# Kernel tuning notes

Measured on AMD Instinct MI355X. Metric: run time of the kernel, lower is better.

## Reference

```python
import jax, jax.numpy as jnp
import numpy as np

EPS = 1e-8
LN_EPS = 1e-5  # torch LayerNorm default


def _l2norm(x):
    # L2-norm along last dim, keepdim, clamped at 1e-8 (matches _l2_norm)
    return jnp.maximum(jnp.sqrt(jnp.sum(x * x, axis=-1, keepdims=True)), 1e-8)


def _ln(x, g, b, n_axes):
    # LayerNorm over the last n_axes dims with elementwise affine
    axes = tuple(range(x.ndim - n_axes, x.ndim))
    mu = jnp.mean(x, axis=axes, keepdims=True)
    var = jnp.var(x, axis=axes, keepdims=True)
    return (x - mu) / jnp.sqrt(var + LN_EPS) * g + b


def _get_zs(x, Wk, bk, Wv, bv, zg, zb, sg, sb):
    z = jax.nn.elu(x @ Wk + bk)                     # (B,L,D)
    v = x @ Wv + bv                                  # (B,L,D)
    s = jnp.einsum('blp,blq->blpq', z, v)            # (B,L,D,D)
    z = jnp.cumsum(z, axis=1)
    s = jnp.cumsum(s, axis=1)
    return _ln(z + EPS, zg, zb, 1), _ln(s + EPS, sg, sb, 2)


def setup_inputs() -> dict:
    key = jax.random.key(0)
    ks = jax.random.split(key, 16)
    B, L, LP, IN, D, NU = 16, 512, 8, 64, 64, 1024
    w = lambda k, sh: (jax.random.normal(k, sh, dtype=jnp.float32) * 0.05)
    inp = {
        'user_id': jax.random.randint(ks[0], (B,), 0, NU),
        'seqs_emb': jax.random.normal(ks[1], (B, L, IN), dtype=jnp.float32),
        'P': jax.random.normal(ks[2], (B, LP, IN), dtype=jnp.float32),
        'S': jax.random.normal(ks[3], (B, LP, IN), dtype=jnp.float32),
        'Wq': w(ks[4], (IN, D)), 'bq': jnp.zeros((D,), jnp.float32),
        'Wk': w(ks[5], (IN, D)), 'bk': jnp.zeros((D,), jnp.float32),
        'Wv': w(ks[6], (IN, D)), 'bv': jnp.zeros((D,), jnp.float32),
        'z_g': jnp.ones((D,), jnp.float32), 'z_b': jnp.zeros((D,), jnp.float32),
        's_g': jnp.ones((D, D), jnp.float32), 's_b': jnp.zeros((D, D), jnp.float32),
        'nam_g': jnp.ones((D, D), jnp.float32), 'nam_b': jnp.zeros((D, D), jnp.float32),
        'na_g': jnp.ones((D,), jnp.float32), 'na_b': jnp.zeros((D,), jnp.float32),
        'prev_z_buf': w(ks[7], (NU + 1, D)),
        'prev_s_buf': w(ks[8], (NU + 1, D, D)),
    }
    return inp


def reference(user_id, seqs_emb, P, S, Wq, bq, Wk, bk, Wv, bv,
              z_g, z_b, s_g, s_b, nam_g, nam_b, na_g, na_b,
              prev_z_buf, prev_s_buf):
    q = jax.nn.elu(seqs_emb @ Wq + bq)                          # (B,L,D)
    z, s = _get_zs(seqs_emb, Wk, bk, Wv, bv, z_g, z_b, s_g, s_b)
    # prompt P: add last-step cumulative state
    P_z, P_s = _get_zs(P, Wk, bk, Wv, bv, z_g, z_b, s_g, s_b)
    z = z + P_z[:, -1:, :]
    s = s + P_s[:, -1:, :, :]
    # CSN path (use_csn=True): q normalized with detached norm
    norm_q = q / jax.lax.stop_gradient(_l2norm(q))
    nam = s / _l2norm(z)[..., None]                             # (B,L,D,D)
    na = jnp.einsum('bld,bldp->blp', norm_q, _ln(nam + EPS, nam_g, nam_b, 2))
    # history path (use_history=True) with prompt S
    S_z, S_s = _get_zs(S, Wk, bk, Wv, bv, z_g, z_b, s_g, s_b)
    prev_z = prev_z_buf[user_id] + S_z[:, -1, :]                # (B,D)
    prev_s = prev_s_buf[user_id] + S_s[:, -1, :, :]             # (B,D,D)
    prev_nam = prev_s / (_l2norm(prev_z)[..., None] + EPS)
    prev_na = jnp.einsum('blp,bpq->blq', norm_q, _ln(prev_nam + EPS, nam_g, nam_b, 2))
    na = na + prev_na  # dropout is identity in eval mode
    na = _ln(na, na_g, na_b, 1)
    # unbiased std over all elements (torch.std default)
    std = jnp.std(q / jnp.maximum(z, 1e-6), ddof=1)
    return na, std
```

## Files before the change

### kernel.cpp

```cpp
#include <hip/hip_runtime.h>
#include <math.h>
#include <stdint.h>

#define B_ 16
#define L_ 512
#define IN_ 64
#define D_ 64
#define LP_ 8

#define LN_EPS 1e-5f
#define EPSF 1e-8f

__device__ __forceinline__ float wredf(float v){
    #pragma unroll
    for (int o = 32; o; o >>= 1) v += __shfl_xor(v, o, 64);
    return v;
}
__device__ __forceinline__ double wredd(double v){
    #pragma unroll
    for (int o = 32; o; o >>= 1) v += __shfl_xor(v, o, 64);
    return v;
}

__device__ __forceinline__ void gl_lds4(const float* gsrc, float* ldst){
    __builtin_amdgcn_global_load_lds((const __attribute__((address_space(1))) void*)gsrc,
                                     (__attribute__((address_space(3))) void*)ldst, 4, 0, 0);
}

template<int LC, int NCH>
__global__ __launch_bounds__(256) void k0_fused(
    const float* __restrict__ X,
    const float* __restrict__ Wq, const float* __restrict__ bq,
    const float* __restrict__ Wk, const float* __restrict__ bk,
    const float* __restrict__ Wv, const float* __restrict__ bv,
    float* __restrict__ Q, float* __restrict__ Z, float* __restrict__ V,
    float* __restrict__ spart, float* __restrict__ zpart,
    double* __restrict__ qstats)
{
    __shared__ float sW[3][IN_*D_];
    __shared__ float sx[4][IN_];
    __shared__ float sz[16][D_], sv[16][D_];
    int t = threadIdx.x;
    if (blockIdx.x == 0 && t < 2) qstats[t] = 0.0;
    for (int i = t; i < IN_*D_; i += 256){ sW[0][i]=Wq[i]; sW[1][i]=Wk[i]; sW[2][i]=Wv[i]; }
    int p = t & 63, g = t >> 6;
    float bqv = bq[p], bkv = bk[p], bvv = bv[p];
    int r0 = blockIdx.x * 16;
    for (int it = 0; it < 4; ++it){
        __syncthreads();
        sx[g][p] = X[(size_t)(r0 + it*4 + g)*IN_ + p];
        __syncthreads();
        int lrow = it*4 + g;
        size_t row = r0 + lrow;
        float aq = bqv, ak = bkv, av = bvv;
        #pragma unroll
        for (int i = 0; i < IN_; i++){
            float x = sx[g][i];
            aq = fmaf(x, sW[0][i*D_+p], aq);
            ak = fmaf(x, sW[1][i*D_+p], ak);
            av = fmaf(x, sW[2][i*D_+p], av);
        }
        aq = aq > 0.f ? aq : (expf(aq)-1.f);
        ak = ak > 0.f ? ak : (expf(ak)-1.f);
        Q[row*D_+p] = aq; Z[row*D_+p] = ak; V[row*D_+p] = av;
        sz[lrow][p] = ak; sv[lrow][p] = av;
    }
    __syncthreads();
    int b = r0 >> 9;
    int c0 = (r0 & 511) / LC;
    #pragma unroll
    for (int ch = 0; ch < NCH; ch++){
        float acc[16];
        #pragma unroll
        for (int i = 0; i < 16; i++) acc[i] = 0.f;
        #pragma unroll
        for (int l = 0; l < LC; l++){
            float vv = sv[ch*LC+l][p];
            #pragma unroll
            for (int i = 0; i < 16; i++) acc[i] = fmaf(sz[ch*LC+l][g*16+i], vv, acc[i]);
        }
        size_t cg = (size_t)(b*(512/LC) + c0 + ch);
        size_t base = cg << 12;
        #pragma unroll
        for (int i = 0; i < 16; i++) spart[base + (g*16+i)*64 + p] = acc[i];
        if (g == 0){
            float za = 0.f;
            #pragma unroll
            for (int l = 0; l < LC; l++) za += sz[ch*LC+l][p];
            zpart[cg*64 + p] = za;
        }
    }
}

__global__ __launch_bounds__(256) void k1_prompt(
    const float* __restrict__ Pm, const float* __restrict__ Sm,
    const float* __restrict__ Wk, const float* __restrict__ bk,
    const float* __restrict__ Wv, const float* __restrict__ bv,
    const float* __restrict__ z_g, const float* __restrict__ z_b,
    const float* __restrict__ s_g, const float* __restrict__ s_b,
    const float* __restrict__ nam_g, const float* __restrict__ nam_b,
    const int* __restrict__ user_id,
    const float* __restrict__ prev_z_buf, const float* __restrict__ prev_s_buf,
    float* __restrict__ Pz, float* __restrict__ Ps, float* __restrict__ prevLN)
{
    __shared__ float sz[LP_][D_], sv[LP_][D_];
    __shared__ double lds[4][2];
    __shared__ float sca[1];
    int blk = blockIdx.x; int b = blk & (B_-1); int path = blk >> 4;
    int t = threadIdx.x, g = t >> 6, p = t & 63;
    const float* Xs = (path ? Sm : Pm) + (size_t)b*LP_*IN_;
    for (int idx = t; idx < 2*LP_*D_; idx += 256){
        int which = idx >> 9;
        int j = (idx >> 6) & 7;
        int d = idx & 63;
        const float* W = which ? Wv : Wk;
        float acc = which ? bv[d] : bk[d];
        const float* xr = Xs + j*IN_;
        #pragma unroll
        for (int i = 0; i < IN_; i++) acc = fmaf(xr[i], W[i*D_+d], acc);
        if (!which) acc = acc > 0.f ? acc : (expf(acc)-1.f);
        if (which) sv[j][d] = acc; else sz[j][d] = acc;
    }
    __syncthreads();
    if (t < 64){
        float zc = 0.f;
        #pragma unroll
        for (int j = 0; j < LP_; j++) zc += sz[j][t];
        double s1 = wredd((double)zc), s2 = wredd((double)zc*(double)zc);
        float mz = (float)(s1*(1.0/64));
        float vz = (float)(s2*(1.0/64) - (s1*(1.0/64))*(s1*(1.0/64)));
        float zf = fmaf((zc-mz)*rsqrtf(vz+LN_EPS), z_g[t], z_b[t]);
        if (path == 0){ Pz[b*D_+t] = zf; }
        else {
            int uid = user_id[b];
            float pz = prev_z_buf[(size_t)uid*D_+t] + zf;
            float rr = wredf(pz*pz);
            if (t == 0) sca[0] = fmaxf(sqrtf(rr), 1e-8f) + EPSF;
        }
    }
    float sc[16];
    #pragma unroll
    for (int i = 0; i < 16; i++){
        int d = g*16 + i; float a = 0.f;
        #pragma unroll
        for (int j = 0; j < LP_; j++) a = fmaf(sz[j][d], sv[j][p], a);
        sc[i] = a;
    }
    double m0 = 0, m1 = 0;
    #pragma unroll
    for (int i = 0; i < 16; i++){ double a = sc[i]; m0 += a; m1 += a*a; }
    m0 = wredd(m0); m1 = wredd(m1);
    __syncthreads();
    if (p == 0){ lds[g][0] = m0; lds[g][1] = m1; }
    __syncthreads();
    m0 = lds[0][0]+lds[1][0]+lds[2][0]+lds[3][0];
    m1 = lds[0][1]+lds[1][1]+lds[2][1]+lds[3][1];
    double mean1 = m0*(1.0/4096.0);
    double var1 = m1*(1.0/4096.0) - mean1*mean1;
    float inv1 = rsqrtf((float)var1 + LN_EPS);
    float mean1f = (float)mean1;
    float sl[16];
    #pragma unroll
    for (int i = 0; i < 16; i++){
        int e = (g*16+i)*D_ + p;
        sl[i] = fmaf((sc[i]-mean1f)*inv1, s_g[e], s_b[e]);
    }
    if (path == 0){
        #pragma unroll
        for (int i = 0; i < 16; i++) Ps[(size_t)b*4096 + (g*16+i)*D_ + p] = sl[i];
        return;
    }
    int uid = user_id[b];
    float denom = sca[0];
    float pn[16]; double n0 = 0, n1 = 0;
    #pragma unroll
    for (int i = 0; i < 16; i++){
        int e = (g*16+i)*D_ + p;
        float ps = prev_s_buf[(size_t)uid*4096 + e] + sl[i];
        float v = ps / denom;
        pn[i] = v; n0 += v; n1 += (double)v*(double)v;
    }
    n0 = wredd(n0); n1 = wredd(n1);
    __syncthreads();
    if (p == 0){ lds[g][0] = n0; lds[g][1] = n1; }
    __syncthreads();
    n0 = lds[0][0]+lds[1][0]+lds[2][0]+lds[3][0];
    n1 = lds[0][1]+lds[1][1]+lds[2][1]+lds[3][1];
    double meanp = n0*(1.0/4096.0);
    double varp = n1*(1.0/4096.0) - meanp*meanp;
    float invp = rsqrtf((float)varp + LN_EPS);
    float meanpf = (float)meanp;
    #pragma unroll
    for (int i = 0; i < 16; i++){
        int e = (g*16+i)*D_ + p;
        prevLN[(size_t)b*4096 + e] = fmaf((pn[i]-meanpf)*invp, nam_g[e], nam_b[e]);
    }
}

template<int C>
__global__ __launch_bounds__(256) void k3_scan(
    float* __restrict__ spart, float* __restrict__ zpart)
{
    int id = blockIdx.x*256 + threadIdx.x;
    const int NS = B_*4096;
    if (id < NS){
        int b = id >> 12, e = id & 4095;
        float a[C];
        #pragma unroll
        for (int c = 0; c < C; c++) a[c] = spart[(((size_t)(b*C+c)) << 12) + e];
        float run = 0.f;
        #pragma unroll
        for (int c = 0; c < C; c++){ float tv = a[c]; a[c] = run; run += tv; }
        #pragma unroll
        for (int c = 0; c < C; c++) spart[(((size_t)(b*C+c)) << 12) + e] = a[c];
    } else if (id < NS + B_*64){
        int k = id - NS;
        int b = k >> 6, d = k & 63;
        float a[C];
        #pragma unroll
        for (int c = 0; c < C; c++) a[c] = zpart[(size_t)(b*C+c)*64 + d];
        float run = 0.f;
        #pragma unroll
        for (int c = 0; c < C; c++){ float tv = a[c]; a[c] = run; run += tv; }
        #pragma unroll
        for (int c = 0; c < C; c++) zpart[(size_t)(b*C+c)*64 + d] = a[c];
    }
}

__global__ __launch_bounds__(256) void k0_qzv(
    const float* __restrict__ X,
    const float* __restrict__ Wq, const float* __restrict__ bq,
    const float* __restrict__ Wk, const float* __restrict__ bk,
    const float* __restrict__ Wv, const float* __restrict__ bv,
    float* __restrict__ Q, float* __restrict__ Z, float* __restrict__ V,
    double* __restrict__ qstats)
{
    __shared__ float sW[3][IN_*D_];
    __shared__ float sx[4][IN_];
    int t = threadIdx.x;
    if (blockIdx.x == 0 && t < 2) qstats[t] = 0.0;
    for (int i = t; i < IN_*D_; i += 256){ sW[0][i]=Wq[i]; sW[1][i]=Wk[i]; sW[2][i]=Wv[i]; }
    int p = t & 63, lr = t >> 6;
    float bqv = bq[p], bkv = bk[p], bvv = bv[p];
    for (int it = 0; it < 4; ++it){
        int r0 = blockIdx.x*16 + it*4;
        __syncthreads();
        for (int i = t; i < 4*IN_; i += 256)
            sx[i>>6][i&63] = X[(size_t)(r0 + (i>>6))*IN_ + (i&63)];
        __syncthreads();
        size_t row = r0 + lr;
        float aq = bqv, ak = bkv, av = bvv;
        #pragma unroll
        for (int i = 0; i < IN_; i++){
            float x = sx[lr][i];
            aq = fmaf(x, sW[0][i*D_+p], aq);
            ak = fmaf(x, sW[1][i*D_+p], ak);
            av = fmaf(x, sW[2][i*D_+p], av);
        }
        Q[row*D_+p] = aq > 0.f ? aq : (expf(aq)-1.f);
        Z[row*D_+p] = ak > 0.f ? ak : (expf(ak)-1.f);
        V[row*D_+p] = av;
    }
}

__global__ __launch_bounds__(256) void k2_chunks(
    const float* __restrict__ Z, const float* __restrict__ V,
    float* __restrict__ spart, float* __restrict__ zpart, int C_, int LC_)
{
    int wg = blockIdx.x; int b = wg / C_, c = wg - b*C_;
    int t = threadIdx.x, g = t >> 6, p = t & 63;
    __shared__ float lz[64], lv[64];
    float acc[16];
    #pragma unroll
    for (int i = 0; i < 16; i++) acc[i] = 0.f;
    float zacc = 0.f;
    for (int l = 0; l < LC_; l++){
        size_t row = (size_t)b*L_ + c*LC_ + l;
        __syncthreads();
        if (t < 64) lz[t] = Z[row*64 + t];
        else if (t < 128) lv[t-64] = V[row*64 + (t-64)];
        __syncthreads();
        float v = lv[p];
        #pragma unroll
        for (int i = 0; i < 16; i++) acc[i] = fmaf(lz[g*16+i], v, acc[i]);
        if (t < 64) zacc += lz[t];
    }
    size_t base = ((size_t)wg) << 12;
    #pragma unroll
    for (int i = 0; i < 16; i++) spart[base + (g*16+i)*64 + p] = acc[i];
    if (t < 64) zpart[(size_t)wg*64 + t] = zacc;
}

__global__ __launch_bounds__(256) void k3_serial(
    float* __restrict__ spart, float* __restrict__ zpart, int C_)
{
    int id = blockIdx.x*256 + threadIdx.x;
    const int NS = B_*4096;
    if (id < NS){
        int b = id >> 12;
        int e = id & 4095;
        float run = 0.f;
        for (int c = 0; c < C_; ++c){
            float* ptr = spart + (((size_t)(b*C_+c)) << 12) + e;
            float tv = *ptr; *ptr = run; run += tv;
        }
    } else if (id < NS + B_*64){
        int k = id - NS;
        int b = k >> 6, d = k & 63;
        float run = 0.f;
        for (int c = 0; c < C_; ++c){
            float* ptr = zpart + (size_t)(b*C_+c)*64 + d;
            float tv = *ptr; *ptr = run; run += tv;
        }
    }
}

__global__ __launch_bounds__(256) void k4_main(
    const float* __restrict__ Q, const float* __restrict__ Z, const float* __restrict__ V,
    const float* __restrict__ spart, const float* __restrict__ zpart,
    const float* __restrict__ Pz, const float* __restrict__ Ps,
    const float* __restrict__ prevLN,
    const float* __restrict__ z_g, const float* __restrict__ z_b,
    const float* __restrict__ s_g, const float* __restrict__ s_b,
    const float* __restrict__ nam_g, const float* __restrict__ nam_b,
    const float* __restrict__ na_g, const float* __restrict__ na_b,
    float* __restrict__ out, double* qstats, int C_, int LC_)
{
    int wg = blockIdx.x; int b = wg / C_, c = wg - b*C_;
    int t = threadIdx.x, g = t >> 6, p = t & 63;
    __shared__ float lz[2][64], lv[2][64], lqb[2][64], lnq[2][64];
    __shared__ float lna[2][4][64];
    __shared__ float lmd[2][4][6];
    __shared__ float lcs[4][5];
    __shared__ float lr[2];
    __shared__ float lPz[64];
    float A[16], Gv[16], Bv[16], NGv[16], NBv[16];
    size_t sbase = ((size_t)wg) << 12;
    size_t bbase = ((size_t)b) << 12;
    size_t row0 = (size_t)b*L_ + (size_t)c*LC_;
    if (g == 1) gl_lds4(Q + row0*64 + p, &lqb[0][0]);
    else if (g == 2) gl_lds4(Z + row0*64 + p, &lz[0][0]);
    else if (g == 3) gl_lds4(V + row0*64 + p, &lv[0][0]);
    #pragma unroll
    for (int i = 0; i < 16; i++){
        int e = (g*16+i)*64 + p;
        A[i]   = spart[sbase + e];
        Gv[i]  = s_g[e];
        Bv[i]  = s_b[e] + Ps[bbase + e];
        NGv[i] = nam_g[e];
        NBv[i] = nam_b[e] + prevLN[bbase + e];
    }
    float cs0=0,cs1=0,cs2=0,cs3=0,cs4=0;
    #pragma unroll
    for (int i = 0; i < 16; i++){
        float gd = Gv[i], bd = Bv[i];
        cs0 += gd; cs1 += gd*gd; cs2 += bd; cs3 += bd*bd; cs4 += gd*bd;
    }
    cs0=wredf(cs0); cs1=wredf(cs1); cs2=wredf(cs2); cs3=wredf(cs3); cs4=wredf(cs4);
    if (p == 0){ lcs[g][0]=cs0; lcs[g][1]=cs1; lcs[g][2]=cs2; lcs[g][3]=cs3; lcs[g][4]=cs4; }
    float zc=0.f, zgr=0.f, zbr=0.f, nagr=0.f, nabr=0.f;
    if (g == 0){
        zc = zpart[(size_t)wg*64 + p];
        lPz[p] = Pz[b*64 + p];
        zgr = z_g[p]; zbr = z_b[p];
    }
    if (g == 3){ nagr = na_g[p]; nabr = na_b[p]; }
    __syncthreads();
    float Cg  = lcs[0][0]+lcs[1][0]+lcs[2][0]+lcs[3][0];
    float Cg2 = lcs[0][1]+lcs[1][1]+lcs[2][1]+lcs[3][1];
    float Cb  = lcs[0][2]+lcs[1][2]+lcs[2][2]+lcs[3][2];
    float Cb2 = lcs[0][3]+lcs[1][3]+lcs[2][3]+lcs[3][3];
    float Cgb = lcs[0][4]+lcs[1][4]+lcs[2][4]+lcs[3][4];

    double qsum = 0.0, qsq = 0.0;
    const float INV = 1.f/4096.f;
    for (int ll = 0; ll < LC_; ++ll){
        int cur = ll & 1, nxt = cur ^ 1, prv = cur ^ 1;
        size_t row = row0 + ll;
        if (ll + 1 < LC_){
            if (g == 1) gl_lds4(Q + (row+1)*64 + p, &lqb[nxt][0]);
            else if (g == 2) gl_lds4(Z + (row+1)*64 + p, &lz[nxt][0]);
            else if (g == 3) gl_lds4(V + (row+1)*64 + p, &lv[nxt][0]);
        }
        if (g == 0){
            float zl = lz[cur][p]; zc += zl;
            float s1 = wredf(zc), s2 = wredf(zc*zc);
            float mz = s1*(1.f/64.f);
            float vz = s2*(1.f/64.f) - mz*mz;
            float zf = fmaf((zc-mz)*rsqrtf(vz+LN_EPS), zgr, zbr) + lPz[p];
            float rr = wredf(zf*zf);
            if (p == 0) lr[cur] = fmaxf(sqrtf(rr), 1e-8f);
            float qvv = lqb[cur][p];
            float qn = qvv / fmaxf(zf, 1e-6f);
            qsum += (double)qn; qsq += (double)qn*(double)qn;
        }
        if (g == 1){
            float qvv = lqb[cur][p];
            float qq = wredf(qvv*qvv);
            lnq[cur][p] = qvv / fmaxf(sqrtf(qq), 1e-8f);
        }
        float m0=0,m1=0,m2=0,m3=0,m4=0,m5=0;
        float vp = lv[cur][p];
        #pragma unroll
        for (int i = 0; i < 16; i++){
            A[i] = fmaf(lz[cur][g*16+i], vp, A[i]);
            float a = A[i];
            m0 += a; m1 = fmaf(a, a, m1);
            float tt = a * Gv[i];
            m2 += tt; m5 = fmaf(tt, tt, m5); m3 = fmaf(tt, Gv[i], m3); m4 = fmaf(tt, Bv[i], m4);
        }
        m0=wredf(m0); m1=wredf(m1); m2=wredf(m2); m3=wredf(m3); m4=wredf(m4); m5=wredf(m5);
        if (p == 0){
            lmd[cur][g][0]=m0; lmd[cur][g][1]=m1; lmd[cur][g][2]=m2;
            lmd[cur][g][3]=m3; lmd[cur][g][4]=m4; lmd[cur][g][5]=m5;
        }
        __syncthreads();
        float M0 = lmd[cur][0][0]+lmd[cur][1][0]+lmd[cur][2][0]+lmd[cur][3][0];
        float M1 = lmd[cur][0][1]+lmd[cur][1][1]+lmd[cur][2][1]+lmd[cur][3][1];
        float M2 = lmd[cur][0][2]+lmd[cur][1][2]+lmd[cur][2][2]+lmd[cur][3][2];
        float M3 = lmd[cur][0][3]+lmd[cur][1][3]+lmd[cur][2][3]+lmd[cur][3][3];
        float M4 = lmd[cur][0][4]+lmd[cur][1][4]+lmd[cur][2][4]+lmd[cur][3][4];
        float M5 = lmd[cur][0][5]+lmd[cur][1][5]+lmd[cur][2][5]+lmd[cur][3][5];
        float meanA = M0*INV;
        float varA  = M1*INV - meanA*meanA;
        float inv1 = rsqrtf(varA + LN_EPS);
        float sum_sf = inv1*(M2 - meanA*Cg) + Cb;
        float ssq_sf = inv1*inv1*(M5 - 2.f*meanA*M3 + meanA*meanA*Cg2)
                     + 2.f*inv1*(M4 - meanA*Cgb) + Cb2;
        float r = lr[cur];
        float invr = 1.f/r;
        float mean_sf = sum_sf*INV;
        float var_sf  = ssq_sf*INV - mean_sf*mean_sf;
        float mean_nam = mean_sf * invr;
        float var_nam  = var_sf * invr * invr;
        float inv2 = rsqrtf(var_nam + LN_EPS);
        float nal = 0.f;
        #pragma unroll
        for (int i = 0; i < 16; i++){
            float sf = fmaf((A[i]-meanA)*inv1, Gv[i], Bv[i]);
            float nm = sf*invr;
            float elem = fmaf((nm-mean_nam)*inv2, NGv[i], NBv[i]);
            nal = fmaf(lnq[cur][g*16+i], elem, nal);
        }
        lna[cur][g][p] = nal;
        if (g == 3 && ll > 0){
            float nt = lna[prv][0][p]+lna[prv][1][p]+lna[prv][2][p]+lna[prv][3][p];
            float s1 = wredf(nt), s2 = wredf(nt*nt);
            float mu = s1*(1.f/64.f);
            float va = s2*(1.f/64.f) - mu*mu;
            out[(row-1)*64 + p] = fmaf((nt-mu)*rsqrtf(va+LN_EPS), nagr, nabr);
        }
    }
    __syncthreads();
    if (g == 3){
        int lastc = (LC_-1) & 1;
        float nt = lna[lastc][0][p]+lna[lastc][1][p]+lna[lastc][2][p]+lna[lastc][3][p];
        float s1 = wredf(nt), s2 = wredf(nt*nt);
        float mu = s1*(1.f/64.f);
        float va = s2*(1.f/64.f) - mu*mu;
        out[(row0+LC_-1)*64 + p] = fmaf((nt-mu)*rsqrtf(va+LN_EPS), nagr, nabr);
    }
    if (g == 0){
        double s = wredd(qsum), s2 = wredd(qsq);
        if (p == 0){
            atomicAdd(&qstats[0], s);
            atomicAdd(&qstats[1], s2);
        }
    }
}

__global__ void k5_std(const double* __restrict__ qstats, float* __restrict__ out, int idx){
    if (threadIdx.x == 0 && blockIdx.x == 0){
        double s = qstats[0], sq = qstats[1];
        const double N = (double)(B_*L_*D_);
        double var = (sq - s*s/N) / (N - 1.0);
        out[idx] = (float)sqrt(var > 0.0 ? var : 0.0);
    }
}

extern "C" void kernel_launch(void* const* d_in, const int* in_sizes, int n_in,
                              void* d_out, int out_size, void* d_ws, size_t ws_size,
                              hipStream_t stream)
{
    (void)in_sizes; (void)n_in;
    const int*   user_id    = (const int*)d_in[0];
    const float* seqs       = (const float*)d_in[1];
    const float* Pm         = (const float*)d_in[2];
    const float* Sm         = (const float*)d_in[3];
    const float* Wq         = (const float*)d_in[4];
    const float* bq         = (const float*)d_in[5];
    const float* Wk         = (const float*)d_in[6];
    const float* bk         = (const float*)d_in[7];
    const float* Wv         = (const float*)d_in[8];
    const float* bv         = (const float*)d_in[9];
    const float* z_g        = (const float*)d_in[10];
    const float* z_b        = (const float*)d_in[11];
    const float* s_g        = (const float*)d_in[12];
    const float* s_b        = (const float*)d_in[13];
    const float* nam_g      = (const float*)d_in[14];
    const float* nam_b      = (const float*)d_in[15];
    const float* na_g       = (const float*)d_in[16];
    const float* na_b       = (const float*)d_in[17];
    const float* prev_z_buf = (const float*)d_in[18];
    const float* prev_s_buf = (const float*)d_in[19];
    float* out = (float*)d_out;

    char* w = (char*)d_ws;
    double* qstats = (double*)w;
    float* Q  = (float*)(w + 16);
    float* Zb = Q  + 524288;
    float* Vb = Zb + 524288;
    float* Pz = Vb + 524288;
    float* Ps = Pz + 1024;
    float* prevLN = Ps + 65536;
    float* spart  = prevLN + 65536;
    size_t fixedBytes = 16 + (size_t)(3*524288 + 1024 + 2*65536)*4;
    int C = 64;
    while (C > 1 && fixedBytes + (size_t)16*C*(4096+64)*4 > ws_size) C >>= 1;
    int LC = 512 / C;
    float* zpart = spart + (size_t)16*C*4096;

    if (C == 64){
        k0_fused<8,2><<<512, 256, 0, stream>>>(seqs, Wq, bq, Wk, bk, Wv, bv,
                                               Q, Zb, Vb, spart, zpart, qstats);
        k1_prompt<<<32, 256, 0, stream>>>(Pm, Sm, Wk, bk, Wv, bv, z_g, z_b, s_g, s_b,
                                          nam_g, nam_b, user_id, prev_z_buf, prev_s_buf,
                                          Pz, Ps, prevLN);
        k3_scan<64><<<(16*4096 + 16*64 + 255)/256, 256, 0, stream>>>(spart, zpart);
    } else if (C == 32){
        k0_fused<16,1><<<512, 256, 0, stream>>>(seqs, Wq, bq, Wk, bk, Wv, bv,
                                                Q, Zb, Vb, spart, zpart, qstats);
        k1_prompt<<<32, 256, 0, stream>>>(Pm, Sm, Wk, bk, Wv, bv, z_g, z_b, s_g, s_b,
                                          nam_g, nam_b, user_id, prev_z_buf, prev_s_buf,
                                          Pz, Ps, prevLN);
        k3_scan<32><<<(16*4096 + 16*64 + 255)/256, 256, 0, stream>>>(spart, zpart);
    } else {
        k0_qzv<<<512, 256, 0, stream>>>(seqs, Wq, bq, Wk, bk, Wv, bv, Q, Zb, Vb, qstats);
        k1_prompt<<<32, 256, 0, stream>>>(Pm, Sm, Wk, bk, Wv, bv, z_g, z_b, s_g, s_b,
                                          nam_g, nam_b, user_id, prev_z_buf, prev_s_buf,
                                          Pz, Ps, prevLN);
        k2_chunks<<<16*C, 256, 0, stream>>>(Zb, Vb, spart, zpart, C, LC);
        k3_serial<<<(16*4096 + 16*64 + 255)/256, 256, 0, stream>>>(spart, zpart, C);
    }
    k4_main<<<16*C, 256, 0, stream>>>(Q, Zb, Vb, spart, zpart, Pz, Ps, prevLN,
                                      z_g, z_b, s_g, s_b, nam_g, nam_b, na_g, na_b,
                                      out, qstats, C, LC);
    k5_std<<<1, 64, 0, stream>>>(qstats, out, out_size - 1);
}
```

Before: 191.9 us.

## Fuse prompt kernel into projection kernel and fold std into specialized main kernel

Merges the prompt/history kernel into the projection kernel as 32 extra blocks, so the two run concurrently and one launch disappears. The projection now computes 4 rows per thread with register accumulators, reusing weights loaded from LDS. A specialized C=64 main kernel computes the LayerNorm moments algebraically from running sums, and its last block, found with an atomic counter, writes the std result, which removes the separate std kernel. It adds atomic counter logic and adds dispatch paths that only cover C=64 and the generic fallback.

```diff
diff --git a/kernel.cpp b/kernel.cpp
--- a/kernel.cpp
+++ b/kernel.cpp
@@ -28,42 +28,153 @@
 }
 
 template<int LC, int NCH>
-__global__ __launch_bounds__(256) void k0_fused(
+__global__ __launch_bounds__(256) void k0k1(
     const float* __restrict__ X,
     const float* __restrict__ Wq, const float* __restrict__ bq,
     const float* __restrict__ Wk, const float* __restrict__ bk,
     const float* __restrict__ Wv, const float* __restrict__ bv,
     float* __restrict__ Q, float* __restrict__ Z, float* __restrict__ V,
     float* __restrict__ spart, float* __restrict__ zpart,
-    double* __restrict__ qstats)
+    double* __restrict__ qstats, unsigned int* __restrict__ cnt,
+    const float* __restrict__ Pm, const float* __restrict__ Sm,
+    const float* __restrict__ z_g, const float* __restrict__ z_b,
+    const float* __restrict__ s_g, const float* __restrict__ s_b,
+    const float* __restrict__ nam_g, const float* __restrict__ nam_b,
+    const int* __restrict__ user_id,
+    const float* __restrict__ prev_z_buf, const float* __restrict__ prev_s_buf,
+    float* __restrict__ Pz, float* __restrict__ Ps, float* __restrict__ prevLN)
 {
     __shared__ float sW[3][IN_*D_];
-    __shared__ float sx[4][IN_];
+    __shared__ float sx[16][IN_];
     __shared__ float sz[16][D_], sv[16][D_];
-    int t = threadIdx.x;
-    if (blockIdx.x == 0 && t < 2) qstats[t] = 0.0;
-    for (int i = t; i < IN_*D_; i += 256){ sW[0][i]=Wq[i]; sW[1][i]=Wk[i]; sW[2][i]=Wv[i]; }
-    int p = t & 63, g = t >> 6;
+    __shared__ double l2d[4][2];
+    __shared__ float sca[1];
+    int bid = blockIdx.x;
+    int t = threadIdx.x, p = t & 63, g = t >> 6;
+
+    if (bid >= 512){
+        int blk = bid - 512; int b = blk & (B_-1); int path = blk >> 4;
+        const float* Xs = (path ? Sm : Pm) + (size_t)b*LP_*IN_;
+        for (int idx = t; idx < 2*LP_*D_; idx += 256){
+            int which = idx >> 9;
+            int j = (idx >> 6) & 7;
+            int d = idx & 63;
+            const float* W = which ? Wv : Wk;
+            float acc = which ? bv[d] : bk[d];
+            const float* xr = Xs + j*IN_;
+            #pragma unroll
+            for (int i = 0; i < IN_; i++) acc = fmaf(xr[i], W[i*D_+d], acc);
+            if (!which) acc = acc > 0.f ? acc : (expf(acc)-1.f);
+            if (which) sv[j][d] = acc; else sz[j][d] = acc;
+        }
+        __syncthreads();
+        if (t < 64){
+            float zc = 0.f;
+            #pragma unroll
+            for (int j = 0; j < LP_; j++) zc += sz[j][t];
+            double s1 = wredd((double)zc), s2 = wredd((double)zc*(double)zc);
+            float mz = (float)(s1*(1.0/64));
+            float vz = (float)(s2*(1.0/64) - (s1*(1.0/64))*(s1*(1.0/64)));
+            float zf = fmaf((zc-mz)*rsqrtf(vz+LN_EPS), z_g[t], z_b[t]);
+            if (path == 0){ Pz[b*D_+t] = zf; }
+            else {
+                int uid = user_id[b];
+                float pz = prev_z_buf[(size_t)uid*D_+t] + zf;
+                float rr = wredf(pz*pz);
+                if (t == 0) sca[0] = fmaxf(sqrtf(rr), 1e-8f) + EPSF;
+            }
+        }
+        float sc[16];
+        #pragma unroll
+        for (int i = 0; i < 16; i++){
+            int d = g*16 + i; float a = 0.f;
+            #pragma unroll
+            for (int j = 0; j < LP_; j++) a = fmaf(sz[j][d], sv[j][p], a);
+            sc[i] = a;
+        }
+        double m0 = 0, m1 = 0;
+        #pragma unroll
+        for (int i = 0; i < 16; i++){ double a = sc[i]; m0 += a; m1 += a*a; }
+        m0 = wredd(m0); m1 = wredd(m1);
+        __syncthreads();
+        if (p == 0){ l2d[g][0] = m0; l2d[g][1] = m1; }
+        __syncthreads();
+        m0 = l2d[0][0]+l2d[1][0]+l2d[2][0]+l2d[3][0];
+        m1 = l2d[0][1]+l2d[1][1]+l2d[2][1]+l2d[3][1];
+        double mean1 = m0*(1.0/4096.0);
+        double var1 = m1*(1.0/4096.0) - mean1*mean1;
+        float inv1 = rsqrtf((float)var1 + LN_EPS);
+        float mean1f = (float)mean1;
+        float sl[16];
+        #pragma unroll
+        for (int i = 0; i < 16; i++){
+            int e = (g*16+i)*D_ + p;
+            sl[i] = fmaf((sc[i]-mean1f)*inv1, s_g[e], s_b[e]);
+        }
+        if (path == 0){
+            #pragma unroll
+            for (int i = 0; i < 16; i++) Ps[(size_t)b*4096 + (g*16+i)*D_ + p] = sl[i];
+            return;
+        }
+        int uid = user_id[b];
+        float denom = sca[0];
+        float pn[16]; double n0 = 0, n1 = 0;
+        #pragma unroll
+        for (int i = 0; i < 16; i++){
+            int e = (g*16+i)*D_ + p;
+            float ps = prev_s_buf[(size_t)uid*4096 + e] + sl[i];
+            float v = ps / denom;
+            pn[i] = v; n0 += v; n1 += (double)v*(double)v;
+        }
+        n0 = wredd(n0); n1 = wredd(n1);
+        __syncthreads();
+        if (p == 0){ l2d[g][0] = n0; l2d[g][1] = n1; }
+        __syncthreads();
+        n0 = l2d[0][0]+l2d[1][0]+l2d[2][0]+l2d[3][0];
+        n1 = l2d[0][1]+l2d[1][1]+l2d[2][1]+l2d[3][1];
+        double meanp = n0*(1.0/4096.0);
+        double varp = n1*(1.0/4096.0) - meanp*meanp;
+        float invp = rsqrtf((float)varp + LN_EPS);
+        float meanpf = (float)meanp;
+        #pragma unroll
+        for (int i = 0; i < 16; i++){
+            int e = (g*16+i)*D_ + p;
+            prevLN[(size_t)b*4096 + e] = fmaf((pn[i]-meanpf)*invp, nam_g[e], nam_b[e]);
+        }
+        return;
+    }
+
+    if (bid == 0){
+        if (t < 2) qstats[t] = 0.0;
+        if (t == 2) *cnt = 0u;
+    }
+    int r0 = bid * 16;
+    for (int k = t; k < IN_*D_; k += 256){ sW[0][k]=Wq[k]; sW[1][k]=Wk[k]; sW[2][k]=Wv[k]; }
+    for (int k = t; k < 16*IN_; k += 256) sx[k>>6][k&63] = X[(size_t)(r0 + (k>>6))*IN_ + (k&63)];
+    __syncthreads();
+    float aq[4], ak[4], av[4];
     float bqv = bq[p], bkv = bk[p], bvv = bv[p];
-    int r0 = blockIdx.x * 16;
-    for (int it = 0; it < 4; ++it){
-        __syncthreads();
-        sx[g][p] = X[(size_t)(r0 + it*4 + g)*IN_ + p];
-        __syncthreads();
-        int lrow = it*4 + g;
+    #pragma unroll
+    for (int r = 0; r < 4; r++){ aq[r]=bqv; ak[r]=bkv; av[r]=bvv; }
+    #pragma unroll
+    for (int i = 0; i < IN_; i++){
+        float wqv = sW[0][i*D_+p], wkv = sW[1][i*D_+p], wvv = sW[2][i*D_+p];
+        #pragma unroll
+        for (int r = 0; r < 4; r++){
+            float x = sx[g*4+r][i];
+            aq[r] = fmaf(x, wqv, aq[r]);
+            ak[r] = fmaf(x, wkv, ak[r]);
+            av[r] = fmaf(x, wvv, av[r]);
+        }
+    }
+    #pragma unroll
+    for (int r = 0; r < 4; r++){
+        int lrow = g*4 + r;
         size_t row = r0 + lrow;
-        float aq = bqv, ak = bkv, av = bvv;
-        #pragma unroll
-        for (int i = 0; i < IN_; i++){
-            float x = sx[g][i];
-            aq = fmaf(x, sW[0][i*D_+p], aq);
-            ak = fmaf(x, sW[1][i*D_+p], ak);
-            av = fmaf(x, sW[2][i*D_+p], av);
-        }
-        aq = aq > 0.f ? aq : (expf(aq)-1.f);
-        ak = ak > 0.f ? ak : (expf(ak)-1.f);
-        Q[row*D_+p] = aq; Z[row*D_+p] = ak; V[row*D_+p] = av;
-        sz[lrow][p] = ak; sv[lrow][p] = av;
+        float q = aq[r] > 0.f ? aq[r] : (expf(aq[r])-1.f);
+        float z = ak[r] > 0.f ? ak[r] : (expf(ak[r])-1.f);
+        Q[row*D_+p] = q; Z[row*D_+p] = z; V[row*D_+p] = av[r];
+        sz[lrow][p] = z; sv[lrow][p] = av[r];
     }
     __syncthreads();
     int b = r0 >> 9;
@@ -89,6 +200,241 @@
             for (int l = 0; l < LC; l++) za += sz[ch*LC+l][p];
             zpart[cg*64 + p] = za;
         }
+    }
+}
+
+template<int C>
+__global__ __launch_bounds__(256) void k3_scan(
+    float* __restrict__ spart, float* __restrict__ zpart)
+{
+    int id = blockIdx.x*256 + threadIdx.x;
+    const int NS = B_*4096;
+    if (id < NS){
+        int b = id >> 12, e = id & 4095;
+        float a[C];
+        #pragma unroll
+        for (int c = 0; c < C; c++) a[c] = spart[(((size_t)(b*C+c)) << 12) + e];
+        float run = 0.f;
+        #pragma unroll
+        for (int c = 0; c < C; c++){ float tv = a[c]; a[c] = run; run += tv; }
+        #pragma unroll
+        for (int c = 0; c < C; c++) spart[(((size_t)(b*C+c)) << 12) + e] = a[c];
+    } else if (id < NS + B_*64){
+        int k = id - NS;
+        int b = k >> 6, d = k & 63;
+        float a[C];
+        #pragma unroll
+        for (int c = 0; c < C; c++) a[c] = zpart[(size_t)(b*C+c)*64 + d];
+        float run = 0.f;
+        #pragma unroll
+        for (int c = 0; c < C; c++){ float tv = a[c]; a[c] = run; run += tv; }
+        #pragma unroll
+        for (int c = 0; c < C; c++) zpart[(size_t)(b*C+c)*64 + d] = a[c];
+    }
+}
+
+__global__ __launch_bounds__(256, 4) void k4_fused(
+    const float* __restrict__ Q, const float* __restrict__ Z, const float* __restrict__ V,
+    const float* __restrict__ spart, const float* __restrict__ zpart,
+    const float* __restrict__ Pz, const float* __restrict__ Ps,
+    const float* __restrict__ prevLN,
+    const float* __restrict__ z_g, const float* __restrict__ z_b,
+    const float* __restrict__ s_g, const float* __restrict__ s_b,
+    const float* __restrict__ nam_g, const float* __restrict__ nam_b,
+    const float* __restrict__ na_g, const float* __restrict__ na_b,
+    float* __restrict__ out, double* __restrict__ qstats,
+    unsigned int* __restrict__ cnt, int outIdx)
+{
+    const int C_ = 64, LC = 8;
+    int wg = blockIdx.x; int b = wg >> 6, c = wg & 63;
+    int t = threadIdx.x, g = t >> 6, p = t & 63;
+    __shared__ float lzall[LC][64], lvall[LC][64], lqall[LC][64];
+    __shared__ float lnqall[LC][64];
+    __shared__ float lnaAll[LC][4][64];
+    __shared__ float lmd[2][4][6];
+    __shared__ float lcs[4][5];
+    __shared__ float lrA[LC];
+    __shared__ double qpart[4][2];
+    float A[16], Gv[16], Bv[16], NGv[16], NBv[16];
+    size_t sbase = ((size_t)wg) << 12;
+    size_t bbase = ((size_t)b) << 12;
+    size_t row0 = (size_t)b*L_ + (size_t)c*LC;
+
+    for (int k = t; k < 3*LC*64; k += 256){
+        int arr = k / (LC*64);
+        int idx = k - arr*(LC*64);
+        int row = idx >> 6, col = idx & 63;
+        float v = (arr==0 ? Z : (arr==1 ? V : Q))[(row0+row)*64 + col];
+        if (arr == 0) lzall[row][col] = v;
+        else if (arr == 1) lvall[row][col] = v;
+        else lqall[row][col] = v;
+    }
+    #pragma unroll
+    for (int i = 0; i < 16; i++){
+        int e = (g*16+i)*64 + p;
+        A[i]   = spart[sbase + e];
+        Gv[i]  = s_g[e];
+        Bv[i]  = s_b[e] + Ps[bbase + e];
+        NGv[i] = nam_g[e];
+        NBv[i] = nam_b[e] + prevLN[bbase + e];
+    }
+    float zcum = zpart[(size_t)wg*64 + p];
+    float zgr = z_g[p], zbr = z_b[p], Pzv = Pz[b*64 + p];
+    __syncthreads();
+
+    {
+        int l0 = 2*g;
+        float zc = zcum;
+        for (int j = 0; j <= l0; j++) zc += lzall[j][p];
+        double qs = 0.0, qs2 = 0.0;
+        #pragma unroll
+        for (int s = 0; s < 2; s++){
+            int l = l0 + s;
+            if (s == 1) zc += lzall[l][p];
+            float s1 = wredf(zc), s2 = wredf(zc*zc);
+            float mz = s1*(1.f/64.f);
+            float vz = s2*(1.f/64.f) - mz*mz;
+            float zf = fmaf((zc-mz)*rsqrtf(vz+LN_EPS), zgr, zbr) + Pzv;
+            float rr = wredf(zf*zf);
+            if (p == 0) lrA[l] = fmaxf(sqrtf(rr), 1e-8f);
+            float qv = lqall[l][p];
+            float qq = wredf(qv*qv);
+            lnqall[l][p] = qv / fmaxf(sqrtf(qq), 1e-8f);
+            float qn = qv / fmaxf(zf, 1e-6f);
+            qs += (double)qn; qs2 += (double)qn*(double)qn;
+        }
+        qs = wredd(qs); qs2 = wredd(qs2);
+        if (p == 0){ qpart[g][0] = qs; qpart[g][1] = qs2; }
+    }
+    {
+        float cs0=0,cs1=0,cs2=0,cs3=0,cs4=0;
+        #pragma unroll
+        for (int i = 0; i < 16; i++){
+            float gd = Gv[i], bd = Bv[i];
+            cs0 += gd; cs1 += gd*gd; cs2 += bd; cs3 += bd*bd; cs4 += gd*bd;
+        }
+        cs0=wredf(cs0); cs1=wredf(cs1); cs2=wredf(cs2); cs3=wredf(cs3); cs4=wredf(cs4);
+        if (p == 0){ lcs[g][0]=cs0; lcs[g][1]=cs1; lcs[g][2]=cs2; lcs[g][3]=cs3; lcs[g][4]=cs4; }
+    }
+    __syncthreads();
+    float Cg  = lcs[0][0]+lcs[1][0]+lcs[2][0]+lcs[3][0];
+    float Cg2 = lcs[0][1]+lcs[1][1]+lcs[2][1]+lcs[3][1];
+    float Cb  = lcs[0][2]+lcs[1][2]+lcs[2][2]+lcs[3][2];
+    float Cb2 = lcs[0][3]+lcs[1][3]+lcs[2][3]+lcs[3][3];
+    float Cgb = lcs[0][4]+lcs[1][4]+lcs[2][4]+lcs[3][4];
+
+    const float INV = 1.f/4096.f;
+    for (int l = 0; l < LC; ++l){
+        int cur = l & 1;
+        float m0=0,m1=0,m2=0,m3=0,m4=0,m5=0;
+        float vp = lvall[l][p];
+        #pragma unroll
+        for (int i = 0; i < 16; i++){
+            A[i] = fmaf(lzall[l][g*16+i], vp, A[i]);
+            float a = A[i];
+            m0 += a; m1 = fmaf(a, a, m1);
+            float tt = a * Gv[i];
+            m2 += tt; m5 = fmaf(tt, tt, m5); m3 = fmaf(tt, Gv[i], m3); m4 = fmaf(tt, Bv[i], m4);
+        }
+        m0=wredf(m0); m1=wredf(m1); m2=wredf(m2); m3=wredf(m3); m4=wredf(m4); m5=wredf(m5);
+        if (p == 0){
+            lmd[cur][g][0]=m0; lmd[cur][g][1]=m1; lmd[cur][g][2]=m2;
+            lmd[cur][g][3]=m3; lmd[cur][g][4]=m4; lmd[cur][g][5]=m5;
+        }
+        __syncthreads();
+        float M0 = lmd[cur][0][0]+lmd[cur][1][0]+lmd[cur][2][0]+lmd[cur][3][0];
+        float M1 = lmd[cur][0][1]+lmd[cur][1][1]+lmd[cur][2][1]+lmd[cur][3][1];
+        float M2 = lmd[cur][0][2]+lmd[cur][1][2]+lmd[cur][2][2]+lmd[cur][3][2];
+        float M3 = lmd[cur][0][3]+lmd[cur][1][3]+lmd[cur][2][3]+lmd[cur][3][3];
+        float M4 = lmd[cur][0][4]+lmd[cur][1][4]+lmd[cur][2][4]+lmd[cur][3][4];
+        float M5 = lmd[cur][0][5]+lmd[cur][1][5]+lmd[cur][2][5]+lmd[cur][3][5];
+        float meanA = M0*INV;
+        float varA  = M1*INV - meanA*meanA;
+        float inv1 = rsqrtf(varA + LN_EPS);
+        float sum_sf = inv1*(M2 - meanA*Cg) + Cb;
+        float ssq_sf = inv1*inv1*(M5 - 2.f*meanA*M3 + meanA*meanA*Cg2)
+                     + 2.f*inv1*(M4 - meanA*Cgb) + Cb2;
+        float invr = 1.f / lrA[l];
+        float mean_sf = sum_sf*INV;
+        float var_sf  = ssq_sf*INV - mean_sf*mean_sf;
+        float mean_nam = mean_sf * invr;
+        float var_nam  = var_sf * invr * invr;
+        float inv2 = rsqrtf(var_nam + LN_EPS);
+        float nal = 0.f;
+        #pragma unroll
+        for (int i = 0; i < 16; i++){
+            float sf = fmaf((A[i]-meanA)*inv1, Gv[i], Bv[i]);
+            float nm = sf*invr;
+            float elem = fmaf((nm-mean_nam)*inv2, NGv[i], NBv[i]);
+            nal = fmaf(lnqall[l][g*16+i], elem, nal);
+        }
+        lnaAll[l][g][p] = nal;
+    }
+    __syncthreads();
+
+    {
+        float nagr = na_g[p], nabr = na_b[p];
+        #pragma unroll
+        for (int s = 0; s < 2; s++){
+            int l = 2*g + s;
+            float nt = lnaAll[l][0][p]+lnaAll[l][1][p]+lnaAll[l][2][p]+lnaAll[l][3][p];
+            float s1 = wredf(nt), s2 = wredf(nt*nt);
+            float mu = s1*(1.f/64.f);
+            float va = s2*(1.f/64.f) - mu*mu;
+            out[(row0+l)*64 + p] = fmaf((nt-mu)*rsqrtf(va+LN_EPS), nagr, nabr);
+        }
+    }
+    if (t == 0){
+        double S  = qpart[0][0]+qpart[1][0]+qpart[2][0]+qpart[3][0];
+        double S2 = qpart[0][1]+qpart[1][1]+qpart[2][1]+qpart[3][1];
+        atomicAdd(&qstats[0], S);
+        atomicAdd(&qstats[1], S2);
+        __threadfence();
+        unsigned int old = atomicAdd(cnt, 1u);
+        if (old == (unsigned int)(B_*C_ - 1)){
+            __threadfence();
+            double sD  = *((volatile double*)&qstats[0]);
+            double sqD = *((volatile double*)&qstats[1]);
+            const double N = (double)(B_*L_*D_);
+            double var = (sqD - sD*sD/N) / (N - 1.0);
+            out[outIdx] = (float)sqrt(var > 0.0 ? var : 0.0);
+        }
+    }
+}
+
+__global__ __launch_bounds__(256) void k0_qzv(
+    const float* __restrict__ X,
+    const float* __restrict__ Wq, const float* __restrict__ bq,
+    const float* __restrict__ Wk, const float* __restrict__ bk,
+    const float* __restrict__ Wv, const float* __restrict__ bv,
+    float* __restrict__ Q, float* __restrict__ Z, float* __restrict__ V,
+    double* __restrict__ qstats)
+{
+    __shared__ float sW[3][IN_*D_];
+    __shared__ float sx[4][IN_];
+    int t = threadIdx.x;
+    if (blockIdx.x == 0 && t < 2) qstats[t] = 0.0;
+    for (int i = t; i < IN_*D_; i += 256){ sW[0][i]=Wq[i]; sW[1][i]=Wk[i]; sW[2][i]=Wv[i]; }
+    int p = t & 63, lr = t >> 6;
+    float bqv = bq[p], bkv = bk[p], bvv = bv[p];
+    for (int it = 0; it < 4; ++it){
+        int r0 = blockIdx.x*16 + it*4;
+        __syncthreads();
+        for (int i = t; i < 4*IN_; i += 256)
+            sx[i>>6][i&63] = X[(size_t)(r0 + (i>>6))*IN_ + (i&63)];
+        __syncthreads();
+        size_t row = r0 + lr;
+        float aq = bqv, ak = bkv, av = bvv;
+        #pragma unroll
+        for (int i = 0; i < IN_; i++){
+            float x = sx[lr][i];
+            aq = fmaf(x, sW[0][i*D_+p], aq);
+            ak = fmaf(x, sW[1][i*D_+p], ak);
+            av = fmaf(x, sW[2][i*D_+p], av);
+        }
+        Q[row*D_+p] = aq > 0.f ? aq : (expf(aq)-1.f);
+        Z[row*D_+p] = ak > 0.f ? ak : (expf(ak)-1.f);
+        V[row*D_+p] = av;
     }
 }
 
@@ -194,72 +540,6 @@
     for (int i = 0; i < 16; i++){
         int e = (g*16+i)*D_ + p;
         prevLN[(size_t)b*4096 + e] = fmaf((pn[i]-meanpf)*invp, nam_g[e], nam_b[e]);
-    }
-}
-
-template<int C>
-__global__ __launch_bounds__(256) void k3_scan(
-    float* __restrict__ spart, float* __restrict__ zpart)
-{
-    int id = blockIdx.x*256 + threadIdx.x;
-    const int NS = B_*4096;
-    if (id < NS){
-        int b = id >> 12, e = id & 4095;
-        float a[C];
-        #pragma unroll
-        for (int c = 0; c < C; c++) a[c] = spart[(((size_t)(b*C+c)) << 12) + e];
-        float run = 0.f;
-        #pragma unroll
-        for (int c = 0; c < C; c++){ float tv = a[c]; a[c] = run; run += tv; }
-        #pragma unroll
-        for (int c = 0; c < C; c++) spart[(((size_t)(b*C+c)) << 12) + e] = a[c];
-    } else if (id < NS + B_*64){
-        int k = id - NS;
-        int b = k >> 6, d = k & 63;
-        float a[C];
-        #pragma unroll
-        for (int c = 0; c < C; c++) a[c] = zpart[(size_t)(b*C+c)*64 + d];
-        float run = 0.f;
-        #pragma unroll
-        for (int c = 0; c < C; c++){ float tv = a[c]; a[c] = run; run += tv; }
-        #pragma unroll
-        for (int c = 0; c < C; c++) zpart[(size_t)(b*C+c)*64 + d] = a[c];
-    }
-}
-
-__global__ __launch_bounds__(256) void k0_qzv(
-    const float* __restrict__ X,
-    const float* __restrict__ Wq, const float* __restrict__ bq,
-    const float* __restrict__ Wk, const float* __restrict__ bk,
-    const float* __restrict__ Wv, const float* __restrict__ bv,
-    float* __restrict__ Q, float* __restrict__ Z, float* __restrict__ V,
-    double* __restrict__ qstats)
-{
-    __shared__ float sW[3][IN_*D_];
-    __shared__ float sx[4][IN_];
-    int t = threadIdx.x;
-    if (blockIdx.x == 0 && t < 2) qstats[t] = 0.0;
-    for (int i = t; i < IN_*D_; i += 256){ sW[0][i]=Wq[i]; sW[1][i]=Wk[i]; sW[2][i]=Wv[i]; }
-    int p = t & 63, lr = t >> 6;
-    float bqv = bq[p], bkv = bk[p], bvv = bv[p];
-    for (int it = 0; it < 4; ++it){
-        int r0 = blockIdx.x*16 + it*4;
-        __syncthreads();
-        for (int i = t; i < 4*IN_; i += 256)
-            sx[i>>6][i&63] = X[(size_t)(r0 + (i>>6))*IN_ + (i&63)];
-        __syncthreads();
-        size_t row = r0 + lr;
-        float aq = bqv, ak = bkv, av = bvv;
-        #pragma unroll
-        for (int i = 0; i < IN_; i++){
-            float x = sx[lr][i];
-            aq = fmaf(x, sW[0][i*D_+p], aq);
-            ak = fmaf(x, sW[1][i*D_+p], ak);
-            av = fmaf(x, sW[2][i*D_+p], av);
-        }
-        Q[row*D_+p] = aq > 0.f ? aq : (expf(aq)-1.f);
-        Z[row*D_+p] = ak > 0.f ? ak : (expf(ak)-1.f);
-        V[row*D_+p] = av;
     }
 }
 
@@ -507,33 +787,30 @@
 
     char* w = (char*)d_ws;
     double* qstats = (double*)w;
-    float* Q  = (float*)(w + 16);
+    unsigned int* cnt = (unsigned int*)(w + 16);
+    float* Q  = (float*)(w + 32);
     float* Zb = Q  + 524288;
     float* Vb = Zb + 524288;
     float* Pz = Vb + 524288;
     float* Ps = Pz + 1024;
     float* prevLN = Ps + 65536;
     float* spart  = prevLN + 65536;
-    size_t fixedBytes = 16 + (size_t)(3*524288 + 1024 + 2*65536)*4;
+    size_t fixedBytes = 32 + (size_t)(3*524288 + 1024 + 2*65536)*4;
     int C = 64;
     while (C > 1 && fixedBytes + (size_t)16*C*(4096+64)*4 > ws_size) C >>= 1;
     int LC = 512 / C;
     float* zpart = spart + (size_t)16*C*4096;
 
     if (C == 64){
-        k0_fused<8,2><<<512, 256, 0, stream>>>(seqs, Wq, bq, Wk, bk, Wv, bv,
-                                               Q, Zb, Vb, spart, zpart, qstats);
-        k1_prompt<<<32, 256, 0, stream>>>(Pm, Sm, Wk, bk, Wv, bv, z_g, z_b, s_g, s_b,
-                                          nam_g, nam_b, user_id, prev_z_buf, prev_s_buf,
-                                          Pz, Ps, prevLN);
+        k0k1<8,2><<<544, 256, 0, stream>>>(seqs, Wq, bq, Wk, bk, Wv, bv,
+                                           Q, Zb, Vb, spart, zpart, qstats, cnt,
+                                           Pm, Sm, z_g, z_b, s_g, s_b, nam_g, nam_b,
+                                           user_id, prev_z_buf, prev_s_buf,
+                                           Pz, Ps, prevLN);
         k3_scan<64><<<(16*4096 + 16*64 + 255)/256, 256, 0, stream>>>(spart, zpart);
-    } else if (C == 32){
-        k0_fused<16,1><<<512, 256, 0, stream>>>(seqs, Wq, bq, Wk, bk, Wv, bv,
-                                                Q, Zb, Vb, spart, zpart, qstats);
-        k1_prompt<<<32, 256, 0, stream>>>(Pm, Sm, Wk, bk, Wv, bv, z_g, z_b, s_g, s_b,
-                                          nam_g, nam_b, user_id, prev_z_buf, prev_s_buf,
-                                          Pz, Ps, prevLN);
-        k3_scan<32><<<(16*4096 + 16*64 + 255)/256, 256, 0, stream>>>(spart, zpart);
+        k4_fused<<<16*64, 256, 0, stream>>>(Q, Zb, Vb, spart, zpart, Pz, Ps, prevLN,
+                                            z_g, z_b, s_g, s_b, nam_g, nam_b, na_g, na_b,
+                                            out, qstats, cnt, out_size - 1);
     } else {
         k0_qzv<<<512, 256, 0, stream>>>(seqs, Wq, bq, Wk, bk, Wv, bv, Q, Zb, Vb, qstats);
         k1_prompt<<<32, 256, 0, stream>>>(Pm, Sm, Wk, bk, Wv, bv, z_g, z_b, s_g, s_b,
@@ -541,9 +818,9 @@
                                           Pz, Ps, prevLN);
         k2_chunks<<<16*C, 256, 0, stream>>>(Zb, Vb, spart, zpart, C, LC);
         k3_serial<<<(16*4096 + 16*64 + 255)/256, 256, 0, stream>>>(spart, zpart, C);
-    }
-    k4_main<<<16*C, 256, 0, stream>>>(Q, Zb, Vb, spart, zpart, Pz, Ps, prevLN,
-                                      z_g, z_b, s_g, s_b, nam_g, nam_b, na_g, na_b,
-                                      out, qstats, C, LC);
-    k5_std<<<1, 64, 0, stream>>>(qstats, out, out_size - 1);
-}
+        k4_main<<<16*C, 256, 0, stream>>>(Q, Zb, Vb, spart, zpart, Pz, Ps, prevLN,
+                                          z_g, z_b, s_g, s_b, nam_g, nam_b, na_g, na_b,
+                                          out, qstats, C, LC);
+        k5_std<<<1, 64, 0, stream>>>(qstats, out, out_size - 1);
+    }
+}
```

After: 205.3 us. 1.07x slower.
